# Kernel optimization log

Hardware: AMD Instinct MI355X
Metric: run time of the kernel (lower is better)

## Reference

```python
import jax, jax.numpy as jnp
import numpy as np

NEG = -9e15  # fill value used by the torch module for invalid band locations


def _sliding_window_attention(q, k, v, w, padding_mask):
    """Banded (Longformer-style) attention.
    q, k, v: [B, H, S, d]; padding_mask: [B, S] (nonzero = valid).
    S must be a multiple of 2*w (matches the no-extra-padding path of the
    original module). Returns context [B, H, S, d].
    """
    B, H, S, d = q.shape
    nb = S // w  # number of query blocks of size w
    # Query blocks: [B, H, nb, w, d]
    q_c = q.reshape(B, H, nb, w, d)
    # Each query block attends to a 3w-wide key/value slab (w halo each side).
    idx = (jnp.arange(nb) * w)[:, None] + jnp.arange(3 * w)[None, :]  # [nb, 3w]
    k_pad = jnp.pad(k, ((0, 0), (0, 0), (w, w), (0, 0)))
    v_pad = jnp.pad(v, ((0, 0), (0, 0), (w, w), (0, 0)))
    k_c = k_pad[:, :, idx, :]  # [B, H, nb, 3w, d]
    v_c = v_pad[:, :, idx, :]  # [B, H, nb, 3w, d]
    # Block scores: [B, H, nb, w, 3w]
    scores3 = jnp.einsum('bhnxd,bhnyd->bhnxy', q_c, k_c)
    # Extract the (2w+1)-wide band: query local x, band offset j -> slab col x+j
    x_idx = jnp.arange(w)[:, None]                     # [w, 1]
    j_idx = x_idx + jnp.arange(2 * w + 1)[None, :]     # [w, 2w+1], values in [0, 3w-1]
    band = scores3[..., x_idx, j_idx]                  # [B, H, nb, w, 2w+1]
    # Validity: global key position i - w + j must lie in [0, S) and be unpadded.
    key_pos = jnp.arange(S).reshape(nb, w)[:, :, None] - w + jnp.arange(2 * w + 1)
    valid = (key_pos >= 0) & (key_pos < S)                       # [nb, w, 2w+1]
    kmask = padding_mask[:, jnp.clip(key_pos, 0, S - 1)] != 0    # [B, nb, w, 2w+1]
    m = valid[None, None] & kmask[:, None]                       # [B, H, nb, w, 2w+1]
    band = jnp.where(m, band, NEG)
    # Original scales by sqrt(q.shape[-1]) == sqrt(head_dim)
    attn = jax.nn.softmax(band / jnp.sqrt(jnp.asarray(d, band.dtype)), axis=-1)
    attn = jnp.where(m, attn, 0.0)  # mirrors the explicit softmax_mask zeroing
    # Scatter band back to slab layout and contract with values.
    attn3 = jnp.zeros_like(scores3).at[..., x_idx, j_idx].set(attn)
    ctx = jnp.einsum('bhnxy,bhnyd->bhnxd', attn3, v_c)
    return ctx.reshape(B, H, S, d)


def setup_inputs() -> dict:
    key = jax.random.key(0)
    k0, k1, k2 = jax.random.split(key, 3)
    B, S, D, E = 2, 4096, 1024, 1024
    x = jax.random.normal(k0, (B, S, D), jnp.float32)
    padding_mask = jnp.ones((B, S), jnp.int32)
    # xavier_uniform like the torch _reset_parameters; biases zero
    s_qkv = (6.0 / (D + 3 * E)) ** 0.5
    Wqkv = jax.random.uniform(k1, (3 * E, D), jnp.float32, -s_qkv, s_qkv)
    bqkv = jnp.zeros((3 * E,), jnp.float32)
    s_o = (6.0 / (E + E)) ** 0.5
    Wo = jax.random.uniform(k2, (E, E), jnp.float32, -s_o, s_o)
    bo = jnp.zeros((E,), jnp.float32)
    return {'x': x, 'padding_mask': padding_mask, 'Wqkv': Wqkv, 'bqkv': bqkv,
            'Wo': Wo, 'bo': bo}


def reference(x, padding_mask, Wqkv, bqkv, Wo, bo):
    B, S, D = x.shape
    E = Wo.shape[0]
    H = 16
    hd = E // H
    w = 512 // 2  # window_size // 2
    qkv = (x @ Wqkv.T + bqkv).reshape(B, S, H, 3, hd)
    q = jnp.transpose(qkv[..., 0, :], (0, 2, 1, 3))  # [B, H, S, hd]
    k = jnp.transpose(qkv[..., 1, :], (0, 2, 1, 3))
    v = jnp.transpose(qkv[..., 2, :], (0, 2, 1, 3))
    ctx = _sliding_window_attention(q, k, v, w, padding_mask)
    out = jnp.transpose(ctx, (0, 2, 1, 3)).reshape(B, S, E)
    return out @ Wo.T + bo
```

## Files before the change

kernel.cpp:

```cpp
#include <hip/hip_runtime.h>
#include <stdint.h>

typedef __attribute__((ext_vector_type(8))) short short8;
typedef __attribute__((ext_vector_type(4))) float f32x4;

__device__ __forceinline__ unsigned short f2bf(float f) {
  unsigned int u = __builtin_bit_cast(unsigned int, f);
  u += 0x7FFFu + ((u >> 16) & 1u);
  return (unsigned short)(u >> 16);
}

#define GLD_LDS16(gp, lp) \
  __builtin_amdgcn_global_load_lds((const __attribute__((address_space(1))) void*)(gp), \
                                   (__attribute__((address_space(3))) void*)(lp), 16, 0, 0)

__global__ __launch_bounds__(256) void cvt_all_kernel(
    const float* __restrict__ x, const float* __restrict__ Wqkv, const float* __restrict__ Wo,
    unsigned short* __restrict__ xb, unsigned short* __restrict__ Wqkvb,
    unsigned short* __restrict__ Wob) {
  int i = blockIdx.x * 256 + threadIdx.x;
  const float* src; unsigned short* dst; int local; float scale = 1.0f;
  if (i < 1048576) { src = x; dst = xb; local = i; }
  else if (i < 1048576 + 393216) {
    local = i - 1048576; src = Wqkv; dst = Wqkvb;
    int row = (local * 8) >> 10;
    if (((row >> 6) % 3) == 0) scale = 0.125f;
  } else { local = i - 1441792; src = Wo; dst = Wob; }
  const float4* s4 = (const float4*)src;
  float4 a = s4[local * 2], b = s4[local * 2 + 1];
  uint4 o;
  o.x = (unsigned)f2bf(a.x * scale) | ((unsigned)f2bf(a.y * scale) << 16);
  o.y = (unsigned)f2bf(a.z * scale) | ((unsigned)f2bf(a.w * scale) << 16);
  o.z = (unsigned)f2bf(b.x * scale) | ((unsigned)f2bf(b.y * scale) << 16);
  o.w = (unsigned)f2bf(b.z * scale) | ((unsigned)f2bf(b.w * scale) << 16);
  *(uint4*)(dst + (size_t)local * 8) = o;
}

template<int EPI>
__global__ __launch_bounds__(256, 2) void gemm_bt(
    const unsigned short* __restrict__ A, const unsigned short* __restrict__ Bw,
    const float* __restrict__ bias, void* o0, void* o1, void* o2,
    int M, int N, int K, int nbc)
{
  __shared__ __align__(16) unsigned short Asm[128 * 64];
  __shared__ __align__(16) unsigned short Bsm[128 * 64];
  int bid = blockIdx.x;
  int bc = bid % nbc, br = bid / nbc;
  int tid = threadIdx.x;
  int lane = tid & 63, w = tid >> 6;
  int l16 = lane & 15, g = lane >> 4;
  int wr = w >> 1, wc = w & 1;
  f32x4 acc[4][4];
  #pragma unroll
  for (int i = 0; i < 4; i++)
    #pragma unroll
    for (int j = 0; j < 4; j++) acc[i][j] = (f32x4){0.f, 0.f, 0.f, 0.f};

  const int nkt = K >> 6;
  for (int kt = 0; kt < nkt; ++kt) {
    __syncthreads();
    #pragma unroll
    for (int r = 0; r < 4; ++r) {
      int idx = tid + 256 * r;
      int row = idx >> 3, s = idx & 7;
      int gofs = ((s ^ (row & 7)) << 3) + (kt << 6);
      GLD_LDS16(A + (size_t)(br * 128 + row) * K + gofs, &Asm[idx << 3]);
      GLD_LDS16(Bw + (size_t)(bc * 128 + row) * K + gofs, &Bsm[idx << 3]);
    }
    __syncthreads();
    #pragma unroll
    for (int kk = 0; kk < 2; ++kk) {
      short8 af[4], bf[4];
      #pragma unroll
      for (int i = 0; i < 4; i++) {
        int rowa = wr * 64 + i * 16 + l16;
        af[i] = *(const short8*)&Asm[(rowa << 6) + ((((kk << 2) + g) ^ (rowa & 7)) << 3)];
        int rowb = wc * 64 + i * 16 + l16;
        bf[i] = *(const short8*)&Bsm[(rowb << 6) + ((((kk << 2) + g) ^ (rowb & 7)) << 3)];
      }
      #pragma unroll
      for (int i = 0; i < 4; i++)
        #pragma unroll
        for (int j = 0; j < 4; j++)
          acc[i][j] = __builtin_amdgcn_mfma_f32_16x16x32_bf16(af[i], bf[j], acc[i][j], 0, 0, 0);
    }
  }
  #pragma unroll
  for (int i = 0; i < 4; i++) {
    #pragma unroll
    for (int j = 0; j < 4; j++) {
      int n = bc * 128 + wc * 64 + j * 16 + l16;
      int m0 = br * 128 + wr * 64 + i * 16 + g * 4;
      if (EPI == 0) {
        int t = (n >> 6) % 3;
        int hh = n / 192, e = n & 63;
        float bval = bias[n]; if (t == 0) bval *= 0.125f;
        int bb = m0 >> 12, s0 = m0 & 4095;
        if (t == 2) {
          unsigned short p0 = f2bf(acc[i][j][0] + bval);
          unsigned short p1 = f2bf(acc[i][j][1] + bval);
          unsigned short p2 = f2bf(acc[i][j][2] + bval);
          unsigned short p3 = f2bf(acc[i][j][3] + bval);
          uint2 pk;
          pk.x = (unsigned)p0 | ((unsigned)p1 << 16);
          pk.y = (unsigned)p2 | ((unsigned)p3 << 16);
          unsigned short* vt = (unsigned short*)o2;
          *(uint2*)&vt[(((size_t)(bb * 16 + hh) * 64 + e) << 12) + s0] = pk;
        } else {
          unsigned short* dst = (unsigned short*)(t == 0 ? o0 : o1);
          #pragma unroll
          for (int jj = 0; jj < 4; jj++)
            dst[((((size_t)(bb * 16 + hh) << 12) + s0 + jj) << 6) + e] = f2bf(acc[i][j][jj] + bval);
        }
      } else {
        float* o = (float*)o0;
        float bval = bias[n];
        #pragma unroll
        for (int jj = 0; jj < 4; jj++)
          o[(size_t)(m0 + jj) * N + n] = acc[i][j][jj] + bval;
      }
    }
  }
}

__global__ __launch_bounds__(512, 4) void attn_kernel(
    const unsigned short* __restrict__ qb, const unsigned short* __restrict__ kb,
    const unsigned short* __restrict__ vtb, const int* __restrict__ pmask,
    unsigned short* __restrict__ ctxb)
{
  const int S = 4096, HD = 64, WIN = 256;
  const float NEG = -1e38f;
  __shared__ __align__(16) unsigned short Ks[2][64 * 64];
  __shared__ __align__(16) unsigned short Vts[2][64 * 64];
  __shared__ __align__(16) unsigned short Ps[8][16 * 64];

  int bid0 = blockIdx.x;
  int bid = (bid0 & 7) * (gridDim.x >> 3) + (bid0 >> 3);
  int qt = bid & 15;
  int bh = bid >> 4;
  int b = bh >> 4, h = bh & 15;

  const unsigned short* Q  = qb + (size_t)bh * S * HD;
  const unsigned short* Kg = kb + (size_t)bh * S * HD;
  const unsigned short* Vt = vtb + (size_t)bh * HD * S;
  const int* pmrow = pmask + (size_t)b * S;

  int tid = threadIdx.x;
  int lane = tid & 63, w = tid >> 6;
  int l16 = lane & 15, g = lane >> 4;

  int q0 = qt * 256;
  int qw = q0 + w * 32;

  short8 qf[2][2];
  #pragma unroll
  for (int qs = 0; qs < 2; ++qs)
    #pragma unroll
    for (int hh = 0; hh < 2; ++hh)
      qf[qs][hh] = *(const short8*)&Q[(size_t)(qw + qs * 16 + l16) * HD + hh * 32 + g * 8];

  f32x4 ctx[2][4];
  #pragma unroll
  for (int qs = 0; qs < 2; ++qs)
    #pragma unroll
    for (int dt = 0; dt < 4; ++dt) ctx[qs][dt] = (f32x4){0.f, 0.f, 0.f, 0.f};
  float lrun[2][4] = {{0.f,0.f,0.f,0.f},{0.f,0.f,0.f,0.f}};

  int kt0 = (q0 - WIN) >> 6; if (kt0 < 0) kt0 = 0;
  int kt1 = (q0 + 255 + WIN) >> 6; if (kt1 > 63) kt1 = 63;
  int nt = kt1 - kt0 + 1;

#define STAGE(BUF, KT) do {                                                       \
    int kb_ = (KT) * 64;                                                          \
    int row_ = tid >> 3, s_ = tid & 7;                                            \
    int c_ = (s_ ^ (row_ & 7)) << 3;                                              \
    GLD_LDS16(Kg + (size_t)(kb_ + row_) * HD + c_, &Ks[BUF][tid << 3]);           \
    GLD_LDS16(Vt + (size_t)row_ * S + kb_ + c_, &Vts[BUF][tid << 3]);             \
  } while (0)

  STAGE(0, kt0);
  asm volatile("s_waitcnt vmcnt(0)" ::: "memory");
  __syncthreads();

  int cur = 0;
  for (int it = 0; it < nt; ++it) {
    int kbase = (kt0 + it) * 64;
    if (it + 1 < nt) STAGE(cur ^ 1, kt0 + it + 1);

    float kbv[4];
    #pragma unroll
    for (int k4 = 0; k4 < 4; ++k4)
      kbv[k4] = (pmrow[kbase + k4 * 16 + l16] != 0) ? 0.f : NEG;

    #pragma unroll
    for (int qs = 0; qs < 2; ++qs) {
      f32x4 sc[4];
      __builtin_amdgcn_s_setprio(1);
      #pragma unroll
      for (int k4 = 0; k4 < 4; ++k4) {
        int krow = k4 * 16 + l16;
        f32x4 s = (f32x4){0.f, 0.f, 0.f, 0.f};
        short8 kf0 = *(const short8*)&Ks[cur][(krow << 6) + ((g ^ (l16 & 7)) << 3)];
        s = __builtin_amdgcn_mfma_f32_16x16x32_bf16(qf[qs][0], kf0, s, 0, 0, 0);
        short8 kf1 = *(const short8*)&Ks[cur][(krow << 6) + (((4 + g) ^ (l16 & 7)) << 3)];
        s = __builtin_amdgcn_mfma_f32_16x16x32_bf16(qf[qs][1], kf1, s, 0, 0, 0);
        sc[k4] = s;
      }
      __builtin_amdgcn_s_setprio(0);

      int qbase = qw + qs * 16 + g * 4;
      #pragma unroll
      for (int k4 = 0; k4 < 4; ++k4) {
        int kg = kbase + k4 * 16 + l16;
        #pragma unroll
        for (int jj = 0; jj < 4; ++jj) {
          int dq = kg - (qbase + jj) + WIN;
          float sv = sc[k4][jj] + kbv[k4];
          sv = ((unsigned)dq <= 2u * WIN) ? sv : NEG;
          float p = __expf(sv);
          lrun[qs][jj] += p;
          int row = g * 4 + jj, col = k4 * 16 + l16;
          Ps[w][(row << 6) + ((((col >> 3) ^ (row & 7)) << 3) | (col & 7))] = f2bf(p);
        }
      }

      asm volatile("s_waitcnt lgkmcnt(0)" ::: "memory");
      __builtin_amdgcn_sched_barrier(0);
      short8 pf0 = *(const short8*)&Ps[w][(l16 << 6) + ((g ^ (l16 & 7)) << 3)];
      short8 pf1 = *(const short8*)&Ps[w][(l16 << 6) + (((4 + g) ^ (l16 & 7)) << 3)];
      __builtin_amdgcn_s_setprio(1);
      #pragma unroll
      for (int dt = 0; dt < 4; ++dt) {
        int drow = dt * 16 + l16;
        short8 vf0 = *(const short8*)&Vts[cur][(drow << 6) + ((g ^ (drow & 7)) << 3)];
        ctx[qs][dt] = __builtin_amdgcn_mfma_f32_16x16x32_bf16(pf0, vf0, ctx[qs][dt], 0, 0, 0);
        short8 vf1 = *(const short8*)&Vts[cur][(drow << 6) + (((4 + g) ^ (drow & 7)) << 3)];
        ctx[qs][dt] = __builtin_amdgcn_mfma_f32_16x16x32_bf16(pf1, vf1, ctx[qs][dt], 0, 0, 0);
      }
      __builtin_amdgcn_s_setprio(0);
    }

    if (it + 1 < nt) {
      asm volatile("s_waitcnt vmcnt(0)" ::: "memory");
      __syncthreads();
      cur ^= 1;
    }
  }
#undef STAGE

  #pragma unroll
  for (int qs = 0; qs < 2; ++qs) {
    #pragma unroll
    for (int jj = 0; jj < 4; ++jj) {
      float ps = lrun[qs][jj];
      #pragma unroll
      for (int mk = 1; mk < 16; mk <<= 1) ps += __shfl_xor(ps, mk);
      float rc = (ps > 0.f) ? (1.f / ps) : 0.f;
      int qrow = qw + qs * 16 + g * 4 + jj;
      size_t base = ((size_t)b * S + qrow) * 1024 + h * 64;
      #pragma unroll
      for (int dt = 0; dt < 4; ++dt)
        ctxb[base + dt * 16 + l16] = f2bf(ctx[qs][dt][jj] * rc);
    }
  }
}

extern "C" void kernel_launch(void* const* d_in, const int* in_sizes, int n_in,
                              void* d_out, int out_size, void* d_ws, size_t ws_size,
                              hipStream_t stream) {
  const float* x     = (const float*)d_in[0];
  const int*   pmask = (const int*)d_in[1];
  const float* Wqkv  = (const float*)d_in[2];
  const float* bqkv  = (const float*)d_in[3];
  const float* Wo    = (const float*)d_in[4];
  const float* bo    = (const float*)d_in[5];

  char* wsp = (char*)d_ws;
  unsigned short* xb    = (unsigned short*)(wsp);
  unsigned short* Wqkvb = (unsigned short*)(wsp + (size_t)(16u << 20));
  unsigned short* Wob   = (unsigned short*)(wsp + (size_t)(22u << 20));
  unsigned short* vtb   = (unsigned short*)(wsp + (size_t)(24u << 20));
  unsigned short* ctxb  = (unsigned short*)(wsp + (size_t)(40u << 20));
  unsigned short* qbuf  = (unsigned short*)d_out;
  unsigned short* kbuf  = (unsigned short*)d_out + (size_t)8388608;

  cvt_all_kernel<<<6144, 256, 0, stream>>>(x, Wqkv, Wo, xb, Wqkvb, Wob);

  gemm_bt<0><<<(8192 / 128) * (3072 / 128), 256, 0, stream>>>(
      xb, Wqkvb, bqkv, qbuf, kbuf, vtb, 8192, 3072, 1024, 3072 / 128);

  attn_kernel<<<512, 512, 0, stream>>>(qbuf, kbuf, vtb, pmask, ctxb);

  gemm_bt<1><<<(8192 / 128) * (1024 / 128), 256, 0, stream>>>(
      ctxb, Wob, bo, d_out, nullptr, nullptr, 8192, 1024, 1024, 1024 / 128);
}
```

Before: 162.9 us.

## Skip out-of-band key tiles per query subtile and use exp2 with folded scale

```diff
diff --git a/kernel.cpp b/kernel.cpp
--- a/kernel.cpp
+++ b/kernel.cpp
@@ -1,13 +1,25 @@
 #include <hip/hip_runtime.h>
+#include <hip/hip_bf16.h>
 #include <stdint.h>
 
 typedef __attribute__((ext_vector_type(8))) short short8;
 typedef __attribute__((ext_vector_type(4))) float f32x4;
+
+#define QSCALE 0.18033688011112042f
 
 __device__ __forceinline__ unsigned short f2bf(float f) {
   unsigned int u = __builtin_bit_cast(unsigned int, f);
   u += 0x7FFFu + ((u >> 16) & 1u);
   return (unsigned short)(u >> 16);
+}
+
+__device__ __forceinline__ unsigned short f2bf_fast(float f) {
+  __hip_bfloat16 h = __float2bfloat16(f);
+  return __builtin_bit_cast(unsigned short, h);
+}
+
+__device__ __forceinline__ float exp2_fast(float x) {
+  float r; asm("v_exp_f32 %0, %1" : "=v"(r) : "v"(x)); return r;
 }
 
 #define GLD_LDS16(gp, lp) \
@@ -24,7 +36,7 @@
   else if (i < 1048576 + 393216) {
     local = i - 1048576; src = Wqkv; dst = Wqkvb;
     int row = (local * 8) >> 10;
-    if (((row >> 6) % 3) == 0) scale = 0.125f;
+    if (((row >> 6) % 3) == 0) scale = QSCALE;
   } else { local = i - 1441792; src = Wo; dst = Wob; }
   const float4* s4 = (const float4*)src;
   float4 a = s4[local * 2], b = s4[local * 2 + 1];
@@ -94,7 +106,7 @@
       if (EPI == 0) {
         int t = (n >> 6) % 3;
         int hh = n / 192, e = n & 63;
-        float bval = bias[n]; if (t == 0) bval *= 0.125f;
+        float bval = bias[n]; if (t == 0) bval *= QSCALE;
         int bb = m0 >> 12, s0 = m0 & 4095;
         if (t == 2) {
           unsigned short p0 = f2bf(acc[i][j][0] + bval);
@@ -187,57 +199,74 @@
     int kbase = (kt0 + it) * 64;
     if (it + 1 < nt) STAGE(cur ^ 1, kt0 + it + 1);
 
-    float kbv[4];
-    #pragma unroll
-    for (int k4 = 0; k4 < 4; ++k4)
-      kbv[k4] = (pmrow[kbase + k4 * 16 + l16] != 0) ? 0.f : NEG;
-
-    #pragma unroll
-    for (int qs = 0; qs < 2; ++qs) {
-      f32x4 sc[4];
-      __builtin_amdgcn_s_setprio(1);
-      #pragma unroll
-      for (int k4 = 0; k4 < 4; ++k4) {
-        int krow = k4 * 16 + l16;
-        f32x4 s = (f32x4){0.f, 0.f, 0.f, 0.f};
-        short8 kf0 = *(const short8*)&Ks[cur][(krow << 6) + ((g ^ (l16 & 7)) << 3)];
-        s = __builtin_amdgcn_mfma_f32_16x16x32_bf16(qf[qs][0], kf0, s, 0, 0, 0);
-        short8 kf1 = *(const short8*)&Ks[cur][(krow << 6) + (((4 + g) ^ (l16 & 7)) << 3)];
-        s = __builtin_amdgcn_mfma_f32_16x16x32_bf16(qf[qs][1], kf1, s, 0, 0, 0);
-        sc[k4] = s;
+    bool any0 = (kbase >= qw - 319) && (kbase <= qw + 271);
+    bool any1 = (kbase >= qw - 303) && (kbase <= qw + 287);
+
+    if (any0 || any1) {
+      float kbv[4];
+      #pragma unroll
+      for (int k4 = 0; k4 < 4; ++k4)
+        kbv[k4] = (pmrow[kbase + k4 * 16 + l16] != 0) ? 0.f : NEG;
+
+      #pragma unroll
+      for (int qs = 0; qs < 2; ++qs) {
+        int Q0 = qw + qs * 16;
+        if (kbase < Q0 - 319 || kbase > Q0 + 271) continue;
+        bool full = (kbase >= Q0 - 241) && (kbase <= Q0 + 193);
+
+        f32x4 sc[4];
+        __builtin_amdgcn_s_setprio(1);
+        #pragma unroll
+        for (int k4 = 0; k4 < 4; ++k4) {
+          int krow = k4 * 16 + l16;
+          f32x4 s = (f32x4){0.f, 0.f, 0.f, 0.f};
+          short8 kf0 = *(const short8*)&Ks[cur][(krow << 6) + ((g ^ (l16 & 7)) << 3)];
+          s = __builtin_amdgcn_mfma_f32_16x16x32_bf16(qf[qs][0], kf0, s, 0, 0, 0);
+          short8 kf1 = *(const short8*)&Ks[cur][(krow << 6) + (((4 + g) ^ (l16 & 7)) << 3)];
+          s = __builtin_amdgcn_mfma_f32_16x16x32_bf16(qf[qs][1], kf1, s, 0, 0, 0);
+          sc[k4] = s;
+        }
+        __builtin_amdgcn_s_setprio(0);
+
+        int qbase = Q0 + g * 4;
+        if (!full) {
+          #pragma unroll
+          for (int k4 = 0; k4 < 4; ++k4) {
+            int kg = kbase + k4 * 16 + l16;
+            #pragma unroll
+            for (int jj = 0; jj < 4; ++jj) {
+              int dq = kg - (qbase + jj) + WIN;
+              sc[k4][jj] = ((unsigned)dq <= 2u * WIN) ? sc[k4][jj] : NEG;
+            }
+          }
+        }
+        #pragma unroll
+        for (int k4 = 0; k4 < 4; ++k4) {
+          int col = k4 * 16 + l16;
+          #pragma unroll
+          for (int jj = 0; jj < 4; ++jj) {
+            float p = exp2_fast(sc[k4][jj] + kbv[k4]);
+            lrun[qs][jj] += p;
+            int row = g * 4 + jj;
+            Ps[w][(row << 6) + ((((col >> 3) ^ (row & 7)) << 3) | (col & 7))] = f2bf_fast(p);
+          }
+        }
+
+        asm volatile("s_waitcnt lgkmcnt(0)" ::: "memory");
+        __builtin_amdgcn_sched_barrier(0);
+        short8 pf0 = *(const short8*)&Ps[w][(l16 << 6) + ((g ^ (l16 & 7)) << 3)];
+        short8 pf1 = *(const short8*)&Ps[w][(l16 << 6) + (((4 + g) ^ (l16 & 7)) << 3)];
+        __builtin_amdgcn_s_setprio(1);
+        #pragma unroll
+        for (int dt = 0; dt < 4; ++dt) {
+          int drow = dt * 16 + l16;
+          short8 vf0 = *(const short8*)&Vts[cur][(drow << 6) + ((g ^ (drow & 7)) << 3)];
+          ctx[qs][dt] = __builtin_amdgcn_mfma_f32_16x16x32_bf16(pf0, vf0, ctx[qs][dt], 0, 0, 0);
+          short8 vf1 = *(const short8*)&Vts[cur][(drow << 6) + (((4 + g) ^ (drow & 7)) << 3)];
+          ctx[qs][dt] = __builtin_amdgcn_mfma_f32_16x16x32_bf16(pf1, vf1, ctx[qs][dt], 0, 0, 0);
+        }
+        __builtin_amdgcn_s_setprio(0);
       }
-      __builtin_amdgcn_s_setprio(0);
-
-      int qbase = qw + qs * 16 + g * 4;
-      #pragma unroll
-      for (int k4 = 0; k4 < 4; ++k4) {
-        int kg = kbase + k4 * 16 + l16;
-        #pragma unroll
-        for (int jj = 0; jj < 4; ++jj) {
-          int dq = kg - (qbase + jj) + WIN;
-          float sv = sc[k4][jj] + kbv[k4];
-          sv = ((unsigned)dq <= 2u * WIN) ? sv : NEG;
-          float p = __expf(sv);
-          lrun[qs][jj] += p;
-          int row = g * 4 + jj, col = k4 * 16 + l16;
-          Ps[w][(row << 6) + ((((col >> 3) ^ (row & 7)) << 3) | (col & 7))] = f2bf(p);
-        }
-      }
-
-      asm volatile("s_waitcnt lgkmcnt(0)" ::: "memory");
-      __builtin_amdgcn_sched_barrier(0);
-      short8 pf0 = *(const short8*)&Ps[w][(l16 << 6) + ((g ^ (l16 & 7)) << 3)];
-      short8 pf1 = *(const short8*)&Ps[w][(l16 << 6) + (((4 + g) ^ (l16 & 7)) << 3)];
-      __builtin_amdgcn_s_setprio(1);
-      #pragma unroll
-      for (int dt = 0; dt < 4; ++dt) {
-        int drow = dt * 16 + l16;
-        short8 vf0 = *(const short8*)&Vts[cur][(drow << 6) + ((g ^ (drow & 7)) << 3)];
-        ctx[qs][dt] = __builtin_amdgcn_mfma_f32_16x16x32_bf16(pf0, vf0, ctx[qs][dt], 0, 0, 0);
-        short8 vf1 = *(const short8*)&Vts[cur][(drow << 6) + (((4 + g) ^ (drow & 7)) << 3)];
-        ctx[qs][dt] = __builtin_amdgcn_mfma_f32_16x16x32_bf16(pf1, vf1, ctx[qs][dt], 0, 0, 0);
-      }
-      __builtin_amdgcn_s_setprio(0);
     }
 
     if (it + 1 < nt) {
```

New measurement: 147.4 us. -9.5%, faster.
